# Optimization experiments

Measured on AMD Instinct MI355X. Metric: run time of the kernel, lower is better.

The kernel has to match this reference:

```python
import jax, jax.numpy as jnp
import numpy as np

K = 8  # args.k


def setup_inputs() -> dict:
    key = jax.random.key(0)
    k1, k2, k3 = jax.random.split(key, 3)
    b, n_pre, n_cur = 1, 8192, 16384
    pre_xyzs = jax.random.normal(k1, (b, 3, n_pre), dtype=jnp.float32)
    cur_xyzs = jax.random.normal(k2, (b, 3, n_cur), dtype=jnp.float32)
    # UpsampleNumLayer output range: sigmoid * (max_upsample_num - 1) + 1  in [1, 8]
    upsample_num = jax.random.uniform(k3, (b, n_pre), dtype=jnp.float32) * 7.0 + 1.0
    return {"pre_xyzs": pre_xyzs, "cur_xyzs": cur_xyzs, "upsample_num": upsample_num}


def _sqdist(a, b):
    # a: (b, n, 3), b: (b, m, 3) -> (b, n, m) squared euclidean distances
    return ((a * a).sum(-1)[:, :, None]
            + (b * b).sum(-1)[:, None, :]
            - 2.0 * jnp.einsum('bnc,bmc->bnm', a, b))


def reference(pre_xyzs, cur_xyzs, upsample_num):
    # pre_xyzs: (b, 3, n_pre); cur_xyzs: (b, 3, n_cur); upsample_num: (b, n_pre)
    pre_t = pre_xyzs.transpose(0, 2, 1)  # (b, n_pre, 3)
    cur_t = cur_xyzs.transpose(0, 2, 1)  # (b, n_cur, 3)

    # knnquery_heap(1, pre, cur): nearest pre index for each cur point -> (b, n_cur)
    cur2pre = jnp.argmin(_sqdist(cur_t, pre_t), axis=-1)

    # knnquery_heap(K, cur, pre): K nearest cur indices for each pre point -> (b, n_pre, K)
    _, knn_idx = jax.lax.top_k(-_sqdist(pre_t, cur_t), K)

    # real_center: gather cur2pre at knn_idx -> (b, n_pre, K)
    real_center = jax.vmap(lambda c2p, idx: c2p[idx])(cur2pre, knn_idx)
    expect_center = jnp.arange(pre_xyzs.shape[2])[None, :, None]  # (1, n_pre, 1)
    mask = (expect_center == real_center).astype(pre_xyzs.dtype)  # (b, n_pre, K)

    # knn_xyzs: gather cur_xyzs columns at knn_idx -> (b, 3, n_pre, K)
    knn_xyzs = jax.vmap(lambda pts, idx: pts[:, idx])(cur_xyzs, knn_idx)

    diff = knn_xyzs - pre_xyzs[..., None]              # (b, 3, n_pre, K)
    dist = jnp.sqrt((diff * diff).sum(axis=1))         # (b, n_pre, K), L2 over channel dim
    mean_distance = (dist * mask).sum(axis=-1) / upsample_num  # (b, n_pre)
    return mean_distance
```

## Files before the change

kernel.cpp:

```cpp
#include <hip/hip_runtime.h>

#define N_PRE 8192
#define N_CUR 16384
#define KNN   8


#define MAPPED_INF 0xFF800000u

__device__ __forceinline__ unsigned key_of(float d) {
    unsigned b = __float_as_uint(d);
    return b ^ (0x80000000u | (unsigned)((int)b >> 31));
}
__device__ __forceinline__ float float_of_key(unsigned k) {
    unsigned b = (k & 0x80000000u) ? (k ^ 0x80000000u) : ~k;
    return __uint_as_float(b);
}
__device__ __forceinline__ unsigned shfl_u32(unsigned x, int src) {
    return (unsigned)__shfl((int)x, src);
}
__device__ __forceinline__ unsigned shfl_up1_u32(unsigned x) {
    return (unsigned)__shfl_up((int)x, 1);
}

__global__ __launch_bounds__(256) void prep_kernel(
        const float* __restrict__ pre, const float* __restrict__ cur,
        float4* __restrict__ pre4, float4* __restrict__ cur4) {
    int i = blockIdx.x * 256 + threadIdx.x;
    if (i < N_CUR) {
        float x = cur[i], y = cur[N_CUR + i], z = cur[2 * N_CUR + i];
        cur4[i] = make_float4(x, y, z, fmaf(x, x, fmaf(y, y, z * z)));
    }
    if (i < N_PRE) {
        float x = pre[i], y = pre[N_PRE + i], z = pre[2 * N_PRE + i];
        pre4[i] = make_float4(-2.f * x, -2.f * y, -2.f * z,
                              fmaf(x, x, fmaf(y, y, z * z)));
    }
}

#define TILE_A 2048

__global__ __launch_bounds__(1024) void cur2pre_kernel(
        const float4* __restrict__ pre4, const float4* __restrict__ cur4,
        unsigned* __restrict__ c2p) {
    __shared__ float4 sp[TILE_A];
    const int tid  = threadIdx.x;
    const int lane = tid & 63;
    const int w    = tid >> 6;
    const int j0   = blockIdx.x * 32 + w * 2;

    const float4 c0 = cur4[j0 + 0];
    const float4 c1 = cur4[j0 + 1];

    const float INF = __int_as_float(0x7F800000);
    float b0 = INF, b1 = INF;
    int   i0 = 0,   i1 = 0;

    for (int tile = 0; tile < N_PRE; tile += TILE_A) {
        __syncthreads();
        for (int k = tid; k < TILE_A; k += 1024) sp[k] = pre4[tile + k];
        __syncthreads();

#pragma unroll 8
        for (int s = 0; s < TILE_A; s += 64) {
            float4 q = sp[s + lane];
            int idx = tile + s + lane;
            float d0 = fmaf(q.x, c0.x, fmaf(q.y, c0.y, fmaf(q.z, c0.z, q.w)));
            float d1 = fmaf(q.x, c1.x, fmaf(q.y, c1.y, fmaf(q.z, c1.z, q.w)));
            if (d0 < b0) { b0 = d0; i0 = idx; }
            if (d1 < b1) { b1 = d1; i1 = idx; }
        }
    }

    float        bs[2] = {b0, b1};
    int          is[2] = {i0, i1};
#pragma unroll
    for (int t = 0; t < 2; ++t) {
        unsigned long long v =
            (((unsigned long long)key_of(bs[t])) << 32) | (unsigned)is[t];
#pragma unroll
        for (int off = 32; off > 0; off >>= 1) {
            unsigned long long o = __shfl_xor((unsigned long long)v, off);
            v = (o < v) ? o : v;
        }
        if (lane == 0) c2p[j0 + t] = (unsigned)(v & 0xFFFFFFFFull);
    }
}

#define TILE_B 2048

__global__ __launch_bounds__(1024) void knn_finalize_kernel(
        const float4* __restrict__ pre4, const float4* __restrict__ cur4,
        const float* __restrict__ ups,
        const unsigned* __restrict__ c2p,
        float* __restrict__ out) {
    __shared__ float4 sc[TILE_B];
    const int tid  = threadIdx.x;
    const int lane = tid & 63;
    const int w    = tid >> 6;
    const int i0   = blockIdx.x * 16 + w;

    const float4 p0 = pre4[i0];

    unsigned ld0 = MAPPED_INF, li0 = 0u;
    float t80 = __int_as_float(0x7F800000);

    for (int tile = 0; tile < N_CUR; tile += TILE_B) {
        __syncthreads();
        for (int k = tid; k < TILE_B; k += 1024) sc[k] = cur4[tile + k];
        __syncthreads();

#pragma unroll 8
        for (int s = 0; s < TILE_B; s += 64) {
            float4 c = sc[s + lane];
            float d0 = fmaf(p0.x, c.x, fmaf(p0.y, c.y, fmaf(p0.z, c.z, c.w)));
            int jj = tile + s + lane;

            unsigned long long m0 = __ballot(d0 < t80);
            while (m0) {
                int src = __ffsll(m0) - 1;
                float fd = __uint_as_float(shfl_u32(__float_as_uint(d0), src));
                unsigned kd = key_of(fd);
                unsigned kj = shfl_u32((unsigned)jj, src);
                unsigned ud = shfl_up1_u32(ld0);
                unsigned uj = shfl_up1_u32(li0);
                if (lane == 0) ud = 0u;
                bool hi = kd < ud, lo = kd < ld0;
                ld0 = hi ? ud : (lo ? kd : ld0);
                li0 = hi ? uj : (lo ? kj : li0);
                t80 = float_of_key(shfl_u32(ld0, 7));
                m0 = (m0 & (m0 - 1)) & __ballot(d0 < t80);
            }
        }
    }

    unsigned j = shfl_u32(li0, lane & 7);

    float contrib = 0.f;
    if (lane < 8) {
        float4 c = cur4[j];
        float px = -0.5f * p0.x;
        float py = -0.5f * p0.y;
        float pz = -0.5f * p0.z;
        float dx = c.x - px, dy = c.y - py, dz = c.z - pz;
        float dsq = fmaf(dx, dx, fmaf(dy, dy, dz * dz));
        unsigned owner = c2p[j];
        contrib = (owner == (unsigned)i0) ? sqrtf(dsq) : 0.f;
    }
    contrib += __shfl_xor(contrib, 1);
    contrib += __shfl_xor(contrib, 2);
    contrib += __shfl_xor(contrib, 4);
    if (lane == 0) out[i0] = contrib / ups[i0];
}

extern "C" void kernel_launch(void* const* d_in, const int* in_sizes, int n_in,
                              void* d_out, int out_size, void* d_ws, size_t ws_size,
                              hipStream_t stream) {
    const float* pre = (const float*)d_in[0];
    const float* cur = (const float*)d_in[1];
    const float* ups = (const float*)d_in[2];
    float* out = (float*)d_out;

    char* ws = (char*)d_ws;
    unsigned* c2p = (unsigned*)ws;
    float4*   pre4 = (float4*)(ws + 65536);
    float4*   cur4 = (float4*)(ws + 65536 + 131072);

    prep_kernel<<<N_CUR / 256, 256, 0, stream>>>(pre, cur, pre4, cur4);

    cur2pre_kernel<<<N_CUR / 32, 1024, 0, stream>>>(pre4, cur4, c2p);

    knn_finalize_kernel<<<N_PRE / 16, 1024, 0, stream>>>(pre4, cur4, ups, c2p, out);
}
```

Before: 139.6 us.

## Register-block multiple queries per wave and drop LDS tiling in both KNN kernels

Both search kernels now have each wavefront handle several query points at once (8 cur points for the nearest-pre search, 4 pre points for the top-8 search). They stream candidates straight from global memory with register prefetch instead of staging them in LDS behind block-wide barriers. The nearest search switches from a per-lane min plus final reduction to a wave-uniform running minimum updated through ballot and readlane. The top-8 insertion uses DPP row shifts and readlane instead of generic shuffles. This is meant to reuse each candidate load across more queries and cut shuffle and sync overhead, at the cost of more registers and serialized ballot loops per query.

```diff
diff --git a/kernel.cpp b/kernel.cpp
--- a/kernel.cpp
+++ b/kernel.cpp
@@ -7,19 +7,12 @@
 
 #define MAPPED_INF 0xFF800000u
 
-__device__ __forceinline__ unsigned key_of(float d) {
-    unsigned b = __float_as_uint(d);
+__device__ __forceinline__ unsigned key_of_bits(unsigned b) {
     return b ^ (0x80000000u | (unsigned)((int)b >> 31));
 }
 __device__ __forceinline__ float float_of_key(unsigned k) {
-    unsigned b = (k & 0x80000000u) ? (k ^ 0x80000000u) : ~k;
+    unsigned b = k ^ (0x80000000u | ~(unsigned)((int)k >> 31));
     return __uint_as_float(b);
-}
-__device__ __forceinline__ unsigned shfl_u32(unsigned x, int src) {
-    return (unsigned)__shfl((int)x, src);
-}
-__device__ __forceinline__ unsigned shfl_up1_u32(unsigned x) {
-    return (unsigned)__shfl_up((int)x, 1);
 }
 
 __global__ __launch_bounds__(256) void prep_kernel(
@@ -37,119 +30,180 @@
     }
 }
 
-#define TILE_A 2048
-
-__global__ __launch_bounds__(1024) void cur2pre_kernel(
+#define Q_A 8
+
+__device__ __forceinline__ void pop_min(float d, float& bf, unsigned& bk,
+                                        unsigned& bi, int sbase) {
+    unsigned long long m = __ballot(d < bf);
+    while (m) {
+        int src = __ffsll(m) - 1;
+        unsigned fdb = (unsigned)__builtin_amdgcn_readlane(__float_as_int(d), src);
+        unsigned kd = key_of_bits(fdb);
+        if (kd < bk) {
+            bk = kd;
+            bi = (unsigned)(sbase + src);
+            bf = __uint_as_float(fdb);
+        }
+        m &= m - 1;
+    }
+}
+
+__global__ __launch_bounds__(256) void cur2pre_kernel(
         const float4* __restrict__ pre4, const float4* __restrict__ cur4,
         unsigned* __restrict__ c2p) {
-    __shared__ float4 sp[TILE_A];
-    const int tid  = threadIdx.x;
-    const int lane = tid & 63;
-    const int w    = tid >> 6;
-    const int j0   = blockIdx.x * 32 + w * 2;
+    const int lane = threadIdx.x & 63;
+    const int wv   = (blockIdx.x * 256 + threadIdx.x) >> 6;
+    const int j0   = wv * Q_A;
 
     const float4 c0 = cur4[j0 + 0];
     const float4 c1 = cur4[j0 + 1];
+    const float4 c2 = cur4[j0 + 2];
+    const float4 c3 = cur4[j0 + 3];
+    const float4 c4 = cur4[j0 + 4];
+    const float4 c5 = cur4[j0 + 5];
+    const float4 c6 = cur4[j0 + 6];
+    const float4 c7 = cur4[j0 + 7];
 
     const float INF = __int_as_float(0x7F800000);
-    float b0 = INF, b1 = INF;
-    int   i0 = 0,   i1 = 0;
-
-    for (int tile = 0; tile < N_PRE; tile += TILE_A) {
-        __syncthreads();
-        for (int k = tid; k < TILE_A; k += 1024) sp[k] = pre4[tile + k];
-        __syncthreads();
-
-#pragma unroll 8
-        for (int s = 0; s < TILE_A; s += 64) {
-            float4 q = sp[s + lane];
-            int idx = tile + s + lane;
-            float d0 = fmaf(q.x, c0.x, fmaf(q.y, c0.y, fmaf(q.z, c0.z, q.w)));
-            float d1 = fmaf(q.x, c1.x, fmaf(q.y, c1.y, fmaf(q.z, c1.z, q.w)));
-            if (d0 < b0) { b0 = d0; i0 = idx; }
-            if (d1 < b1) { b1 = d1; i1 = idx; }
-        }
-    }
-
-    float        bs[2] = {b0, b1};
-    int          is[2] = {i0, i1};
-#pragma unroll
-    for (int t = 0; t < 2; ++t) {
-        unsigned long long v =
-            (((unsigned long long)key_of(bs[t])) << 32) | (unsigned)is[t];
-#pragma unroll
-        for (int off = 32; off > 0; off >>= 1) {
-            unsigned long long o = __shfl_xor((unsigned long long)v, off);
-            v = (o < v) ? o : v;
-        }
-        if (lane == 0) c2p[j0 + t] = (unsigned)(v & 0xFFFFFFFFull);
-    }
-}
-
-#define TILE_B 2048
-
-__global__ __launch_bounds__(1024) void knn_finalize_kernel(
+    float    bf0 = INF, bf1 = INF, bf2 = INF, bf3 = INF,
+             bf4 = INF, bf5 = INF, bf6 = INF, bf7 = INF;
+    unsigned bk0 = 0xFFFFFFFFu, bk1 = bk0, bk2 = bk0, bk3 = bk0,
+             bk4 = bk0, bk5 = bk0, bk6 = bk0, bk7 = bk0;
+    unsigned bi0 = 0, bi1 = 0, bi2 = 0, bi3 = 0,
+             bi4 = 0, bi5 = 0, bi6 = 0, bi7 = 0;
+
+#define PROC_A(qv, sb)                                                        \
+    {                                                                         \
+        float d0 = fmaf(qv.x, c0.x, fmaf(qv.y, c0.y, fmaf(qv.z, c0.z, qv.w))); \
+        float d1 = fmaf(qv.x, c1.x, fmaf(qv.y, c1.y, fmaf(qv.z, c1.z, qv.w))); \
+        float d2 = fmaf(qv.x, c2.x, fmaf(qv.y, c2.y, fmaf(qv.z, c2.z, qv.w))); \
+        float d3 = fmaf(qv.x, c3.x, fmaf(qv.y, c3.y, fmaf(qv.z, c3.z, qv.w))); \
+        float d4 = fmaf(qv.x, c4.x, fmaf(qv.y, c4.y, fmaf(qv.z, c4.z, qv.w))); \
+        float d5 = fmaf(qv.x, c5.x, fmaf(qv.y, c5.y, fmaf(qv.z, c5.z, qv.w))); \
+        float d6 = fmaf(qv.x, c6.x, fmaf(qv.y, c6.y, fmaf(qv.z, c6.z, qv.w))); \
+        float d7 = fmaf(qv.x, c7.x, fmaf(qv.y, c7.y, fmaf(qv.z, c7.z, qv.w))); \
+        pop_min(d0, bf0, bk0, bi0, sb);                                       \
+        pop_min(d1, bf1, bk1, bi1, sb);                                       \
+        pop_min(d2, bf2, bk2, bi2, sb);                                       \
+        pop_min(d3, bf3, bk3, bi3, sb);                                       \
+        pop_min(d4, bf4, bk4, bi4, sb);                                       \
+        pop_min(d5, bf5, bk5, bi5, sb);                                       \
+        pop_min(d6, bf6, bk6, bi6, sb);                                       \
+        pop_min(d7, bf7, bk7, bi7, sb);                                       \
+    }
+
+    float4 qa = pre4[lane];
+    float4 qb = pre4[64 + lane];
+    for (int s = 0; s < N_PRE; s += 128) {
+        float4 qn0 = pre4[((s + 128) & (N_PRE - 1)) + lane];
+        float4 qn1 = pre4[((s + 192) & (N_PRE - 1)) + lane];
+        PROC_A(qa, s);
+        PROC_A(qb, s + 64);
+        qa = qn0;
+        qb = qn1;
+    }
+#undef PROC_A
+
+    unsigned ov = bi0;
+    ov = (lane == 1) ? bi1 : ov;
+    ov = (lane == 2) ? bi2 : ov;
+    ov = (lane == 3) ? bi3 : ov;
+    ov = (lane == 4) ? bi4 : ov;
+    ov = (lane == 5) ? bi5 : ov;
+    ov = (lane == 6) ? bi6 : ov;
+    ov = (lane == 7) ? bi7 : ov;
+    if (lane < 8) c2p[j0 + lane] = ov;
+}
+
+#define P_B 4
+
+__device__ __forceinline__ void pop_top8(float d, float& t8, unsigned& ld,
+                                         unsigned& li, int sbase) {
+    unsigned long long m = __ballot(d < t8);
+    while (m) {
+        int src = __ffsll(m) - 1;
+        unsigned fdb = (unsigned)__builtin_amdgcn_readlane(__float_as_int(d), src);
+        unsigned kd = key_of_bits(fdb);
+        unsigned kj = (unsigned)(sbase + src);
+        unsigned ud = (unsigned)__builtin_amdgcn_update_dpp(
+            0, (int)ld, 0x111, 0xF, 0xF, false);
+        unsigned uj = (unsigned)__builtin_amdgcn_update_dpp(
+            0, (int)li, 0x111, 0xF, 0xF, false);
+        bool hi = kd < ud;
+        bool lo = kd < ld;
+        ld = hi ? ud : (lo ? kd : ld);
+        li = hi ? uj : (lo ? kj : li);
+        unsigned k7 = (unsigned)__builtin_amdgcn_readlane((int)ld, 7);
+        t8 = float_of_key(k7);
+        m = (m & (m - 1)) & __ballot(d < t8);
+    }
+}
+
+__global__ __launch_bounds__(256) void knn_finalize_kernel(
         const float4* __restrict__ pre4, const float4* __restrict__ cur4,
         const float* __restrict__ ups,
         const unsigned* __restrict__ c2p,
         float* __restrict__ out) {
-    __shared__ float4 sc[TILE_B];
-    const int tid  = threadIdx.x;
-    const int lane = tid & 63;
-    const int w    = tid >> 6;
-    const int i0   = blockIdx.x * 16 + w;
-
-    const float4 p0 = pre4[i0];
-
-    unsigned ld0 = MAPPED_INF, li0 = 0u;
-    float t80 = __int_as_float(0x7F800000);
-
-    for (int tile = 0; tile < N_CUR; tile += TILE_B) {
-        __syncthreads();
-        for (int k = tid; k < TILE_B; k += 1024) sc[k] = cur4[tile + k];
-        __syncthreads();
-
-#pragma unroll 8
-        for (int s = 0; s < TILE_B; s += 64) {
-            float4 c = sc[s + lane];
-            float d0 = fmaf(p0.x, c.x, fmaf(p0.y, c.y, fmaf(p0.z, c.z, c.w)));
-            int jj = tile + s + lane;
-
-            unsigned long long m0 = __ballot(d0 < t80);
-            while (m0) {
-                int src = __ffsll(m0) - 1;
-                float fd = __uint_as_float(shfl_u32(__float_as_uint(d0), src));
-                unsigned kd = key_of(fd);
-                unsigned kj = shfl_u32((unsigned)jj, src);
-                unsigned ud = shfl_up1_u32(ld0);
-                unsigned uj = shfl_up1_u32(li0);
-                if (lane == 0) ud = 0u;
-                bool hi = kd < ud, lo = kd < ld0;
-                ld0 = hi ? ud : (lo ? kd : ld0);
-                li0 = hi ? uj : (lo ? kj : li0);
-                t80 = float_of_key(shfl_u32(ld0, 7));
-                m0 = (m0 & (m0 - 1)) & __ballot(d0 < t80);
-            }
-        }
-    }
-
-    unsigned j = shfl_u32(li0, lane & 7);
-
-    float contrib = 0.f;
-    if (lane < 8) {
-        float4 c = cur4[j];
-        float px = -0.5f * p0.x;
-        float py = -0.5f * p0.y;
-        float pz = -0.5f * p0.z;
-        float dx = c.x - px, dy = c.y - py, dz = c.z - pz;
-        float dsq = fmaf(dx, dx, fmaf(dy, dy, dz * dz));
-        unsigned owner = c2p[j];
-        contrib = (owner == (unsigned)i0) ? sqrtf(dsq) : 0.f;
-    }
-    contrib += __shfl_xor(contrib, 1);
-    contrib += __shfl_xor(contrib, 2);
-    contrib += __shfl_xor(contrib, 4);
-    if (lane == 0) out[i0] = contrib / ups[i0];
+    const int lane = threadIdx.x & 63;
+    const int wv   = (blockIdx.x * 256 + threadIdx.x) >> 6;
+    const int i0   = wv * P_B;
+
+    const float4 p0 = pre4[i0 + 0];
+    const float4 p1 = pre4[i0 + 1];
+    const float4 p2 = pre4[i0 + 2];
+    const float4 p3 = pre4[i0 + 3];
+
+    const float INF = __int_as_float(0x7F800000);
+    unsigned ld0 = MAPPED_INF, li0 = 0, ld1 = MAPPED_INF, li1 = 0;
+    unsigned ld2 = MAPPED_INF, li2 = 0, ld3 = MAPPED_INF, li3 = 0;
+    float t0 = INF, t1 = INF, t2 = INF, t3 = INF;
+
+#define PROC_B(cv, sb)                                                        \
+    {                                                                         \
+        float d0 = fmaf(p0.x, cv.x, fmaf(p0.y, cv.y, fmaf(p0.z, cv.z, cv.w))); \
+        float d1 = fmaf(p1.x, cv.x, fmaf(p1.y, cv.y, fmaf(p1.z, cv.z, cv.w))); \
+        float d2 = fmaf(p2.x, cv.x, fmaf(p2.y, cv.y, fmaf(p2.z, cv.z, cv.w))); \
+        float d3 = fmaf(p3.x, cv.x, fmaf(p3.y, cv.y, fmaf(p3.z, cv.z, cv.w))); \
+        pop_top8(d0, t0, ld0, li0, sb);                                       \
+        pop_top8(d1, t1, ld1, li1, sb);                                       \
+        pop_top8(d2, t2, ld2, li2, sb);                                       \
+        pop_top8(d3, t3, ld3, li3, sb);                                       \
+    }
+
+    float4 ca = cur4[lane];
+    float4 cb = cur4[64 + lane];
+    for (int s = 0; s < N_CUR; s += 128) {
+        float4 cn0 = cur4[((s + 128) & (N_CUR - 1)) + lane];
+        float4 cn1 = cur4[((s + 192) & (N_CUR - 1)) + lane];
+        PROC_B(ca, s);
+        PROC_B(cb, s + 64);
+        ca = cn0;
+        cb = cn1;
+    }
+#undef PROC_B
+
+#define FIN_B(pp, lip, off)                                                   \
+    {                                                                         \
+        float acc = 0.f;                                                      \
+        if (lane < 8) {                                                       \
+            unsigned j = lip;                                                 \
+            float4 cc = cur4[j];                                              \
+            float px = -0.5f * pp.x, py = -0.5f * pp.y, pz = -0.5f * pp.z;    \
+            float dx = cc.x - px, dy = cc.y - py, dz = cc.z - pz;             \
+            float dsq = fmaf(dx, dx, fmaf(dy, dy, dz * dz));                  \
+            acc = (c2p[j] == (unsigned)(i0 + off)) ? sqrtf(dsq) : 0.f;        \
+        }                                                                     \
+        acc += __shfl_xor(acc, 1);                                            \
+        acc += __shfl_xor(acc, 2);                                            \
+        acc += __shfl_xor(acc, 4);                                            \
+        if (lane == 0) out[i0 + off] = acc / ups[i0 + off];                   \
+    }
+
+    FIN_B(p0, li0, 0)
+    FIN_B(p1, li1, 1)
+    FIN_B(p2, li2, 2)
+    FIN_B(p3, li3, 3)
+#undef FIN_B
 }
 
 extern "C" void kernel_launch(void* const* d_in, const int* in_sizes, int n_in,
@@ -167,7 +221,7 @@
 
     prep_kernel<<<N_CUR / 256, 256, 0, stream>>>(pre, cur, pre4, cur4);
 
-    cur2pre_kernel<<<N_CUR / 32, 1024, 0, stream>>>(pre4, cur4, c2p);
-
-    knn_finalize_kernel<<<N_PRE / 16, 1024, 0, stream>>>(pre4, cur4, ups, c2p, out);
-}
+    cur2pre_kernel<<<N_CUR / (Q_A * 4), 256, 0, stream>>>(pre4, cur4, c2p);
+
+    knn_finalize_kernel<<<N_PRE / (P_B * 4), 256, 0, stream>>>(pre4, cur4, ups, c2p, out);
+}
```

Result: slower. 197.2 us (+41.2%).

## Register-block 8 queries per wave in cur2pre and 2 per wave in top-k

Applied to the files above, without the earlier changes.

The nearest-pre kernel now has each wave handle 8 cur points and drops shared memory. Pre points are streamed straight from global/L2 with a register double-buffer, so each loaded point is reused across 8 queries. The top-k kernel processes two pre points per wave with 512-thread blocks, which halves the shared-tile loads per query. Its insertion loop now uses readlane and DPP row shifts instead of general shuffles. The extra register blocking raises VGPR pressure and may reduce occupancy.

```diff
diff --git a/kernel.cpp b/kernel.cpp
--- a/kernel.cpp
+++ b/kernel.cpp
@@ -7,19 +7,12 @@
 
 #define MAPPED_INF 0xFF800000u
 
-__device__ __forceinline__ unsigned key_of(float d) {
-    unsigned b = __float_as_uint(d);
+__device__ __forceinline__ unsigned key_of_bits(unsigned b) {
     return b ^ (0x80000000u | (unsigned)((int)b >> 31));
 }
 __device__ __forceinline__ float float_of_key(unsigned k) {
-    unsigned b = (k & 0x80000000u) ? (k ^ 0x80000000u) : ~k;
+    unsigned b = k ^ (0x80000000u | ~(unsigned)((int)k >> 31));
     return __uint_as_float(b);
-}
-__device__ __forceinline__ unsigned shfl_u32(unsigned x, int src) {
-    return (unsigned)__shfl((int)x, src);
-}
-__device__ __forceinline__ unsigned shfl_up1_u32(unsigned x) {
-    return (unsigned)__shfl_up((int)x, 1);
 }
 
 __global__ __launch_bounds__(256) void prep_kernel(
@@ -37,58 +30,126 @@
     }
 }
 
-#define TILE_A 2048
-
-__global__ __launch_bounds__(1024) void cur2pre_kernel(
+#define Q_A 8
+
+__global__ __launch_bounds__(256) void cur2pre_kernel(
         const float4* __restrict__ pre4, const float4* __restrict__ cur4,
         unsigned* __restrict__ c2p) {
-    __shared__ float4 sp[TILE_A];
-    const int tid  = threadIdx.x;
-    const int lane = tid & 63;
-    const int w    = tid >> 6;
-    const int j0   = blockIdx.x * 32 + w * 2;
+    const int lane = threadIdx.x & 63;
+    const int wv   = (blockIdx.x * 256 + threadIdx.x) >> 6;
+    const int j0   = wv * Q_A;
 
     const float4 c0 = cur4[j0 + 0];
     const float4 c1 = cur4[j0 + 1];
+    const float4 c2 = cur4[j0 + 2];
+    const float4 c3 = cur4[j0 + 3];
+    const float4 c4 = cur4[j0 + 4];
+    const float4 c5 = cur4[j0 + 5];
+    const float4 c6 = cur4[j0 + 6];
+    const float4 c7 = cur4[j0 + 7];
 
     const float INF = __int_as_float(0x7F800000);
-    float b0 = INF, b1 = INF;
-    int   i0 = 0,   i1 = 0;
-
-    for (int tile = 0; tile < N_PRE; tile += TILE_A) {
-        __syncthreads();
-        for (int k = tid; k < TILE_A; k += 1024) sp[k] = pre4[tile + k];
-        __syncthreads();
-
-#pragma unroll 8
-        for (int s = 0; s < TILE_A; s += 64) {
-            float4 q = sp[s + lane];
-            int idx = tile + s + lane;
-            float d0 = fmaf(q.x, c0.x, fmaf(q.y, c0.y, fmaf(q.z, c0.z, q.w)));
-            float d1 = fmaf(q.x, c1.x, fmaf(q.y, c1.y, fmaf(q.z, c1.z, q.w)));
-            if (d0 < b0) { b0 = d0; i0 = idx; }
-            if (d1 < b1) { b1 = d1; i1 = idx; }
-        }
-    }
-
-    float        bs[2] = {b0, b1};
-    int          is[2] = {i0, i1};
+    float b0 = INF, b1 = INF, b2 = INF, b3 = INF,
+          b4 = INF, b5 = INF, b6 = INF, b7 = INF;
+    int   i0 = 0, i1 = 0, i2 = 0, i3 = 0, i4 = 0, i5 = 0, i6 = 0, i7 = 0;
+
+#define STEP_A(qv, sb)                                                         \
+    {                                                                          \
+        int idxv = (sb) + lane;                                                \
+        float d; bool c;                                                       \
+        d = fmaf(qv.x, c0.x, fmaf(qv.y, c0.y, fmaf(qv.z, c0.z, qv.w)));        \
+        c = d < b0; b0 = c ? d : b0; i0 = c ? idxv : i0;                       \
+        d = fmaf(qv.x, c1.x, fmaf(qv.y, c1.y, fmaf(qv.z, c1.z, qv.w)));        \
+        c = d < b1; b1 = c ? d : b1; i1 = c ? idxv : i1;                       \
+        d = fmaf(qv.x, c2.x, fmaf(qv.y, c2.y, fmaf(qv.z, c2.z, qv.w)));        \
+        c = d < b2; b2 = c ? d : b2; i2 = c ? idxv : i2;                       \
+        d = fmaf(qv.x, c3.x, fmaf(qv.y, c3.y, fmaf(qv.z, c3.z, qv.w)));        \
+        c = d < b3; b3 = c ? d : b3; i3 = c ? idxv : i3;                       \
+        d = fmaf(qv.x, c4.x, fmaf(qv.y, c4.y, fmaf(qv.z, c4.z, qv.w)));        \
+        c = d < b4; b4 = c ? d : b4; i4 = c ? idxv : i4;                       \
+        d = fmaf(qv.x, c5.x, fmaf(qv.y, c5.y, fmaf(qv.z, c5.z, qv.w)));        \
+        c = d < b5; b5 = c ? d : b5; i5 = c ? idxv : i5;                       \
+        d = fmaf(qv.x, c6.x, fmaf(qv.y, c6.y, fmaf(qv.z, c6.z, qv.w)));        \
+        c = d < b6; b6 = c ? d : b6; i6 = c ? idxv : i6;                       \
+        d = fmaf(qv.x, c7.x, fmaf(qv.y, c7.y, fmaf(qv.z, c7.z, qv.w)));        \
+        c = d < b7; b7 = c ? d : b7; i7 = c ? idxv : i7;                       \
+    }
+
+    float4 qa = pre4[lane];
+    float4 qb = pre4[64 + lane];
+    for (int s = 0; s < N_PRE; s += 128) {
+        float4 qn0 = pre4[((s + 128) & (N_PRE - 1)) + lane];
+        float4 qn1 = pre4[((s + 192) & (N_PRE - 1)) + lane];
+        STEP_A(qa, s);
+        STEP_A(qb, s + 64);
+        qa = qn0;
+        qb = qn1;
+    }
+#undef STEP_A
+
+    unsigned long long v0 = (((unsigned long long)key_of_bits(__float_as_uint(b0))) << 32) | (unsigned)i0;
+    unsigned long long v1 = (((unsigned long long)key_of_bits(__float_as_uint(b1))) << 32) | (unsigned)i1;
+    unsigned long long v2 = (((unsigned long long)key_of_bits(__float_as_uint(b2))) << 32) | (unsigned)i2;
+    unsigned long long v3 = (((unsigned long long)key_of_bits(__float_as_uint(b3))) << 32) | (unsigned)i3;
+    unsigned long long v4 = (((unsigned long long)key_of_bits(__float_as_uint(b4))) << 32) | (unsigned)i4;
+    unsigned long long v5 = (((unsigned long long)key_of_bits(__float_as_uint(b5))) << 32) | (unsigned)i5;
+    unsigned long long v6 = (((unsigned long long)key_of_bits(__float_as_uint(b6))) << 32) | (unsigned)i6;
+    unsigned long long v7 = (((unsigned long long)key_of_bits(__float_as_uint(b7))) << 32) | (unsigned)i7;
 #pragma unroll
-    for (int t = 0; t < 2; ++t) {
-        unsigned long long v =
-            (((unsigned long long)key_of(bs[t])) << 32) | (unsigned)is[t];
+    for (int off = 32; off > 0; off >>= 1) {
+        unsigned long long o;
+        o = __shfl_xor(v0, off); v0 = (o < v0) ? o : v0;
+        o = __shfl_xor(v1, off); v1 = (o < v1) ? o : v1;
+        o = __shfl_xor(v2, off); v2 = (o < v2) ? o : v2;
+        o = __shfl_xor(v3, off); v3 = (o < v3) ? o : v3;
+        o = __shfl_xor(v4, off); v4 = (o < v4) ? o : v4;
+        o = __shfl_xor(v5, off); v5 = (o < v5) ? o : v5;
+        o = __shfl_xor(v6, off); v6 = (o < v6) ? o : v6;
+    }
+    {
 #pragma unroll
         for (int off = 32; off > 0; off >>= 1) {
-            unsigned long long o = __shfl_xor((unsigned long long)v, off);
-            v = (o < v) ? o : v;
-        }
-        if (lane == 0) c2p[j0 + t] = (unsigned)(v & 0xFFFFFFFFull);
-    }
+            unsigned long long o = __shfl_xor(v7, off);
+            v7 = (o < v7) ? o : v7;
+        }
+    }
+
+    unsigned r = (unsigned)v0;
+    r = (lane == 1) ? (unsigned)v1 : r;
+    r = (lane == 2) ? (unsigned)v2 : r;
+    r = (lane == 3) ? (unsigned)v3 : r;
+    r = (lane == 4) ? (unsigned)v4 : r;
+    r = (lane == 5) ? (unsigned)v5 : r;
+    r = (lane == 6) ? (unsigned)v6 : r;
+    r = (lane == 7) ? (unsigned)v7 : r;
+    if (lane < 8) c2p[j0 + lane] = r;
 }
 
 #define TILE_B 2048
 
-__global__ __launch_bounds__(1024) void knn_finalize_kernel(
+__device__ __forceinline__ void pop_top8(float d, float& t8, unsigned& ld,
+                                         unsigned& li, int jbase) {
+    unsigned long long m = __ballot(d < t8);
+    while (m) {
+        int src = __ffsll(m) - 1;
+        unsigned fdb = (unsigned)__builtin_amdgcn_readlane(__float_as_int(d), src);
+        unsigned kd = key_of_bits(fdb);
+        unsigned kj = (unsigned)(jbase + src);
+        unsigned ud = (unsigned)__builtin_amdgcn_update_dpp(
+            0, (int)ld, 0x111, 0xF, 0xF, false);
+        unsigned uj = (unsigned)__builtin_amdgcn_update_dpp(
+            0, (int)li, 0x111, 0xF, 0xF, false);
+        bool hi = kd < ud;
+        bool lo = kd < ld;
+        ld = hi ? ud : (lo ? kd : ld);
+        li = hi ? uj : (lo ? kj : li);
+        unsigned k7 = (unsigned)__builtin_amdgcn_readlane((int)ld, 7);
+        t8 = float_of_key(k7);
+        m = (m & (m - 1)) & __ballot(d < t8);
+    }
+}
+
+__global__ __launch_bounds__(512) void knn_finalize_kernel(
         const float4* __restrict__ pre4, const float4* __restrict__ cur4,
         const float* __restrict__ ups,
         const unsigned* __restrict__ c2p,
@@ -97,59 +158,62 @@
     const int tid  = threadIdx.x;
     const int lane = tid & 63;
     const int w    = tid >> 6;
-    const int i0   = blockIdx.x * 16 + w;
-
-    const float4 p0 = pre4[i0];
-
-    unsigned ld0 = MAPPED_INF, li0 = 0u;
-    float t80 = __int_as_float(0x7F800000);
+    const int ia   = blockIdx.x * 16 + w * 2;
+    const int ib   = ia + 1;
+
+    const float4 p0 = pre4[ia];
+    const float4 p1 = pre4[ib];
+
+    const float INF = __int_as_float(0x7F800000);
+    unsigned ld0 = MAPPED_INF, li0 = 0, ld1 = MAPPED_INF, li1 = 0;
+    float t80 = INF, t81 = INF;
 
     for (int tile = 0; tile < N_CUR; tile += TILE_B) {
         __syncthreads();
-        for (int k = tid; k < TILE_B; k += 1024) sc[k] = cur4[tile + k];
+        for (int k = tid; k < TILE_B; k += 512) sc[k] = cur4[tile + k];
         __syncthreads();
 
-#pragma unroll 8
+#pragma unroll 4
         for (int s = 0; s < TILE_B; s += 64) {
             float4 c = sc[s + lane];
             float d0 = fmaf(p0.x, c.x, fmaf(p0.y, c.y, fmaf(p0.z, c.z, c.w)));
-            int jj = tile + s + lane;
-
-            unsigned long long m0 = __ballot(d0 < t80);
-            while (m0) {
-                int src = __ffsll(m0) - 1;
-                float fd = __uint_as_float(shfl_u32(__float_as_uint(d0), src));
-                unsigned kd = key_of(fd);
-                unsigned kj = shfl_u32((unsigned)jj, src);
-                unsigned ud = shfl_up1_u32(ld0);
-                unsigned uj = shfl_up1_u32(li0);
-                if (lane == 0) ud = 0u;
-                bool hi = kd < ud, lo = kd < ld0;
-                ld0 = hi ? ud : (lo ? kd : ld0);
-                li0 = hi ? uj : (lo ? kj : li0);
-                t80 = float_of_key(shfl_u32(ld0, 7));
-                m0 = (m0 & (m0 - 1)) & __ballot(d0 < t80);
-            }
-        }
-    }
-
-    unsigned j = shfl_u32(li0, lane & 7);
-
-    float contrib = 0.f;
-    if (lane < 8) {
-        float4 c = cur4[j];
-        float px = -0.5f * p0.x;
-        float py = -0.5f * p0.y;
-        float pz = -0.5f * p0.z;
-        float dx = c.x - px, dy = c.y - py, dz = c.z - pz;
-        float dsq = fmaf(dx, dx, fmaf(dy, dy, dz * dz));
-        unsigned owner = c2p[j];
-        contrib = (owner == (unsigned)i0) ? sqrtf(dsq) : 0.f;
-    }
-    contrib += __shfl_xor(contrib, 1);
-    contrib += __shfl_xor(contrib, 2);
-    contrib += __shfl_xor(contrib, 4);
-    if (lane == 0) out[i0] = contrib / ups[i0];
+            float d1 = fmaf(p1.x, c.x, fmaf(p1.y, c.y, fmaf(p1.z, c.z, c.w)));
+            const int jbase = tile + s;
+            pop_top8(d0, t80, ld0, li0, jbase);
+            pop_top8(d1, t81, ld1, li1, jbase);
+        }
+    }
+
+    {
+        float acc = 0.f;
+        if (lane < 8) {
+            unsigned j = li0;
+            float4 cc = cur4[j];
+            float px = -0.5f * p0.x, py = -0.5f * p0.y, pz = -0.5f * p0.z;
+            float dx = cc.x - px, dy = cc.y - py, dz = cc.z - pz;
+            float dsq = fmaf(dx, dx, fmaf(dy, dy, dz * dz));
+            acc = (c2p[j] == (unsigned)ia) ? sqrtf(dsq) : 0.f;
+        }
+        acc += __shfl_xor(acc, 1);
+        acc += __shfl_xor(acc, 2);
+        acc += __shfl_xor(acc, 4);
+        if (lane == 0) out[ia] = acc / ups[ia];
+    }
+    {
+        float acc = 0.f;
+        if (lane < 8) {
+            unsigned j = li1;
+            float4 cc = cur4[j];
+            float px = -0.5f * p1.x, py = -0.5f * p1.y, pz = -0.5f * p1.z;
+            float dx = cc.x - px, dy = cc.y - py, dz = cc.z - pz;
+            float dsq = fmaf(dx, dx, fmaf(dy, dy, dz * dz));
+            acc = (c2p[j] == (unsigned)ib) ? sqrtf(dsq) : 0.f;
+        }
+        acc += __shfl_xor(acc, 1);
+        acc += __shfl_xor(acc, 2);
+        acc += __shfl_xor(acc, 4);
+        if (lane == 0) out[ib] = acc / ups[ib];
+    }
 }
 
 extern "C" void kernel_launch(void* const* d_in, const int* in_sizes, int n_in,
@@ -167,7 +231,7 @@
 
     prep_kernel<<<N_CUR / 256, 256, 0, stream>>>(pre, cur, pre4, cur4);
 
-    cur2pre_kernel<<<N_CUR / 32, 1024, 0, stream>>>(pre4, cur4, c2p);
-
-    knn_finalize_kernel<<<N_PRE / 16, 1024, 0, stream>>>(pre4, cur4, ups, c2p, out);
-}
+    cur2pre_kernel<<<N_CUR / (Q_A * 4), 256, 0, stream>>>(pre4, cur4, c2p);
+
+    knn_finalize_kernel<<<N_PRE / 16, 512, 0, stream>>>(pre4, cur4, ups, c2p, out);
+}
```

Result: slower. 155.4 us (+11.3%).
